# Kernel optimization log

Measured on AMD Instinct MI355X. Metric: run time of the kernel, lower is better.

Reference implementation:

```python
import jax, jax.numpy as jnp
import numpy as np
import math

SIGMA = 5.0
N_BINS = 360
B = 65536

def setup_inputs() -> dict:
    key = jax.random.key(0)
    k1, k2 = jax.random.split(key)
    y_pred = jax.random.normal(k1, (B, N_BINS), dtype=jnp.float32)
    y_labels = jax.random.randint(k2, (B,), 0, N_BINS, dtype=jnp.int64 if jax.config.jax_enable_x64 else jnp.int32)
    return {"y_pred": y_pred, "y_labels": y_labels}

def reference(y_pred, y_labels):
    sigma = SIGMA
    x = jnp.arange(N_BINS, dtype=y_pred.dtype)  # [360]
    lbl = y_labels.astype(y_pred.dtype)[:, None]  # [B,1]
    norm = 1.0 / (math.sqrt(2.0 * math.pi) * sigma)
    # Gaussian target distribution centered at each label angle
    y_dist = jnp.exp(-((x[None, :] - lbl) ** 2) / (2.0 * sigma * sigma)) * norm  # [B,360]
    # per-sample squared-error sum over bins, then mean over batch
    return jnp.mean(jnp.sum(jnp.square(y_dist - y_pred), axis=1), axis=0)
```

## Files before the change

### kernel.cpp

```cpp
#include <hip/hip_runtime.h>
#include <math.h>

#define N_BINS 360
#define VEC4_PER_ROW 90

__global__ void __launch_bounds__(256) emd_partial_kernel(
    const float* __restrict__ y_pred,
    const int*   __restrict__ y_labels,
    float*       __restrict__ partials,
    int total_vec4)
{
    const float norm   = 0.07978845608028654f;
    const float inv2s2 = 0.02f;

    float acc = 0.0f;
    const int stride = gridDim.x * blockDim.x;
    const float4* __restrict__ pred4 = reinterpret_cast<const float4*>(y_pred);

    for (int f = blockIdx.x * blockDim.x + threadIdx.x; f < total_vec4; f += stride) {
        const int row = f / VEC4_PER_ROW;
        const int b0  = (f - row * VEC4_PER_ROW) * 4;
        const float lbl = (float)y_labels[row];

        const float4 p = pred4[f];
        float pv[4] = {p.x, p.y, p.z, p.w};
        #pragma unroll
        for (int j = 0; j < 4; ++j) {
            const float t = (float)(b0 + j) - lbl;
            const float e = __expf(-t * t * inv2s2) * norm;
            const float d = e - pv[j];
            acc = fmaf(d, d, acc);
        }
    }

    #pragma unroll
    for (int off = 32; off > 0; off >>= 1)
        acc += __shfl_down(acc, off, 64);

    __shared__ float wsum[4];
    const int wave = threadIdx.x >> 6;
    const int lane = threadIdx.x & 63;
    if (lane == 0) wsum[wave] = acc;
    __syncthreads();
    if (threadIdx.x == 0)
        partials[blockIdx.x] = wsum[0] + wsum[1] + wsum[2] + wsum[3];
}

__global__ void __launch_bounds__(256) emd_final_kernel(
    const float* __restrict__ partials,
    int n,
    float* __restrict__ out,
    double invB)
{
    double acc = 0.0;
    for (int i = threadIdx.x; i < n; i += blockDim.x)
        acc += (double)partials[i];

    __shared__ double sd[256];
    sd[threadIdx.x] = acc;
    __syncthreads();
    #pragma unroll
    for (int s = 128; s > 0; s >>= 1) {
        if (threadIdx.x < s) sd[threadIdx.x] += sd[threadIdx.x + s];
        __syncthreads();
    }
    if (threadIdx.x == 0)
        out[0] = (float)(sd[0] * invB);
}

extern "C" void kernel_launch(void* const* d_in, const int* in_sizes, int n_in,
                              void* d_out, int out_size, void* d_ws, size_t ws_size,
                              hipStream_t stream)
{
    const float* y_pred   = (const float*)d_in[0];
    const int*   y_labels = (const int*)d_in[1];
    float* out = (float*)d_out;

    const int B = in_sizes[1];
    const int total_vec4 = B * VEC4_PER_ROW;

    float* partials = (float*)d_ws;

    const int block = 256;
    int grid = (total_vec4 + block - 1) / block;
    if (grid > 2048) grid = 2048;

    emd_partial_kernel<<<grid, block, 0, stream>>>(y_pred, y_labels, partials, total_vec4);
    emd_final_kernel<<<1, block, 0, stream>>>(partials, grid, out, 1.0 / (double)B);
}
```

Measured before the change: 23.68 us.

## Fuse final reduction into main kernel via last-block atomic counter

Replaces the two-kernel reduction with one kernel. Each block writes its partial sum and increments a global atomic counter, and the last block to finish sums all partials and writes the output. This removes the second kernel launch and its dependency gap, but adds a hipMemsetAsync to reset the counter before each call, plus atomic traffic at block exit.

```diff
diff --git a/kernel.cpp b/kernel.cpp
--- a/kernel.cpp
+++ b/kernel.cpp
@@ -3,12 +3,16 @@
 
 #define N_BINS 360
 #define VEC4_PER_ROW 90
+#define GRID_BLOCKS 2048
 
-__global__ void __launch_bounds__(256) emd_partial_kernel(
+__global__ void __launch_bounds__(256) emd_fused_kernel(
     const float* __restrict__ y_pred,
     const int*   __restrict__ y_labels,
     float*       __restrict__ partials,
-    int total_vec4)
+    unsigned int* __restrict__ counter,
+    float*       __restrict__ out,
+    int total_vec4,
+    float invB)
 {
     const float norm   = 0.07978845608028654f;
     const float inv2s2 = 0.02f;
@@ -23,10 +27,11 @@
         const float lbl = (float)y_labels[row];
 
         const float4 p = pred4[f];
-        float pv[4] = {p.x, p.y, p.z, p.w};
+        const float pv[4] = {p.x, p.y, p.z, p.w};
+        const float tbase = (float)b0 - lbl;
         #pragma unroll
         for (int j = 0; j < 4; ++j) {
-            const float t = (float)(b0 + j) - lbl;
+            const float t = tbase + (float)j;
             const float e = __expf(-t * t * inv2s2) * norm;
             const float d = e - pv[j];
             acc = fmaf(d, d, acc);
@@ -38,34 +43,39 @@
         acc += __shfl_down(acc, off, 64);
 
     __shared__ float wsum[4];
+    __shared__ int lastFlag;
     const int wave = threadIdx.x >> 6;
     const int lane = threadIdx.x & 63;
     if (lane == 0) wsum[wave] = acc;
     __syncthreads();
-    if (threadIdx.x == 0)
-        partials[blockIdx.x] = wsum[0] + wsum[1] + wsum[2] + wsum[3];
-}
 
-__global__ void __launch_bounds__(256) emd_final_kernel(
-    const float* __restrict__ partials,
-    int n,
-    float* __restrict__ out,
-    double invB)
-{
-    double acc = 0.0;
-    for (int i = threadIdx.x; i < n; i += blockDim.x)
-        acc += (double)partials[i];
+    if (threadIdx.x == 0) {
+        const float blocksum = wsum[0] + wsum[1] + wsum[2] + wsum[3];
+        __hip_atomic_store(&partials[blockIdx.x], blocksum,
+                           __ATOMIC_RELAXED, __HIP_MEMORY_SCOPE_AGENT);
+        const unsigned prev = __hip_atomic_fetch_add(counter, 1u,
+                           __ATOMIC_ACQ_REL, __HIP_MEMORY_SCOPE_AGENT);
+        lastFlag = (prev == gridDim.x - 1) ? 1 : 0;
+    }
+    __syncthreads();
 
-    __shared__ double sd[256];
-    sd[threadIdx.x] = acc;
-    __syncthreads();
-    #pragma unroll
-    for (int s = 128; s > 0; s >>= 1) {
-        if (threadIdx.x < s) sd[threadIdx.x] += sd[threadIdx.x + s];
+    if (lastFlag) {
+        double a = 0.0;
+        for (int i = threadIdx.x; i < (int)gridDim.x; i += blockDim.x)
+            a += (double)__hip_atomic_load(&partials[i],
+                           __ATOMIC_RELAXED, __HIP_MEMORY_SCOPE_AGENT);
+
+        __shared__ double sd[256];
+        sd[threadIdx.x] = a;
         __syncthreads();
+        #pragma unroll
+        for (int s = 128; s > 0; s >>= 1) {
+            if (threadIdx.x < s) sd[threadIdx.x] += sd[threadIdx.x + s];
+            __syncthreads();
+        }
+        if (threadIdx.x == 0)
+            out[0] = (float)(sd[0] * (double)invB);
     }
-    if (threadIdx.x == 0)
-        out[0] = (float)(sd[0] * invB);
 }
 
 extern "C" void kernel_launch(void* const* d_in, const int* in_sizes, int n_in,
@@ -80,11 +90,11 @@
     const int total_vec4 = B * VEC4_PER_ROW;
 
     float* partials = (float*)d_ws;
+    unsigned int* counter = (unsigned int*)((char*)d_ws + GRID_BLOCKS * sizeof(float));
 
-    const int block = 256;
-    int grid = (total_vec4 + block - 1) / block;
-    if (grid > 2048) grid = 2048;
+    hipMemsetAsync(counter, 0, sizeof(unsigned int), stream);
 
-    emd_partial_kernel<<<grid, block, 0, stream>>>(y_pred, y_labels, partials, total_vec4);
-    emd_final_kernel<<<1, block, 0, stream>>>(partials, grid, out, 1.0 / (double)B);
+    emd_fused_kernel<<<GRID_BLOCKS, 256, 0, stream>>>(
+        y_pred, y_labels, partials, counter, out,
+        total_vec4, 1.0f / (float)B);
 }
```

After: 76.01 us. 221% more time.
